# Kernel optimization log

Measured on AMD Instinct MI355X. Metric: run time of the kernel, lower is better.

Reference implementation:

```python
import jax, jax.numpy as jnp
import numpy as np

B, T, H, UNITS = 64, 512, 1024, 1024

def setup_inputs() -> dict:
    key = jax.random.key(0)
    ks = jax.random.split(key, 8)
    s = 0.02
    return {
        "dec_hidden": jax.random.normal(ks[0], (B, H), jnp.float32),
        "enc_output": jax.random.normal(ks[1], (B, T, H), jnp.float32),
        "Wh": jax.random.normal(ks[2], (H, UNITS), jnp.float32) * s,
        "bh": jnp.zeros((UNITS,), jnp.float32),
        "Ws": jax.random.normal(ks[3], (H, UNITS), jnp.float32) * s,
        "bs": jnp.zeros((UNITS,), jnp.float32),
        "Wv": jax.random.normal(ks[4], (UNITS, 1), jnp.float32) * s,
        "bv": jnp.zeros((1,), jnp.float32),
    }

def reference(dec_hidden, enc_output, Wh, bh, Ws, bs, Wv, bv):
    # Faithful to original: tanh applied only to W_h(enc_output) term.
    enc_proj = jnp.tanh(jnp.einsum('bth,hu->btu', enc_output, Wh) + bh)  # [B,T,U]
    dec_proj = (dec_hidden @ Ws + bs)[:, None, :]                        # [B,1,U]
    score = jnp.einsum('btu,uo->bto', enc_proj + dec_proj, Wv) + bv      # [B,T,1]
    attn_dist = jax.nn.softmax(score, axis=1)                            # [B,T,1]
    context_vector = jnp.sum(attn_dist * enc_output, axis=1)             # [B,H]
    return context_vector, jnp.squeeze(attn_dist, axis=-1)
```

## Files before the change

### kernel.cpp

```cpp
#include <hip/hip_runtime.h>
#include <hip/hip_bf16.h>

typedef unsigned short u16;
typedef __attribute__((ext_vector_type(8))) short short8;
typedef __attribute__((ext_vector_type(4))) float f32x4;

#define B_  64
#define T_  512
#define H_  1024
#define U_  1024
#define BT_ (B_*T_)

#define BM 128
#define BN 128
#define BK 32

#define GLL16(gp, lp) __builtin_amdgcn_global_load_lds( \
    (const __attribute__((address_space(1))) void*)(gp), \
    (__attribute__((address_space(3))) void*)(lp), 16, 0, 0)

__device__ __forceinline__ u16 f32_to_bf16(float f) {
  union { float f; unsigned u; } v; v.f = f;
  unsigned r = v.u + 0x7FFFu + ((v.u >> 16) & 1u);
  return (u16)(r >> 16);
}
__device__ __forceinline__ unsigned pack_bf16x2(float lo, float hi) {
  return (unsigned)f32_to_bf16(lo) | ((unsigned)f32_to_bf16(hi) << 16);
}

__global__ __launch_bounds__(256) void ba_conv_enc(const float4* __restrict__ in,
                                                   uint4* __restrict__ out) {
  int i = blockIdx.x * 256 + threadIdx.x;
  float4 v0 = in[2 * i], v1 = in[2 * i + 1];
  uint4 o;
  o.x = pack_bf16x2(v0.x, v0.y);
  o.y = pack_bf16x2(v0.z, v0.w);
  o.z = pack_bf16x2(v1.x, v1.y);
  o.w = pack_bf16x2(v1.z, v1.w);
  out[i] = o;
}

__global__ __launch_bounds__(256) void ba_conv_whT(const float* __restrict__ wh,
                                                   u16* __restrict__ whT) {
  __shared__ float tile[32][33];
  int tx = threadIdx.x, ty = threadIdx.y;
  int u0 = blockIdx.x * 32, h0 = blockIdx.y * 32;
  #pragma unroll
  for (int i = 0; i < 32; i += 8)
    tile[ty + i][tx] = wh[(long)(h0 + ty + i) * U_ + u0 + tx];
  __syncthreads();
  #pragma unroll
  for (int i = 0; i < 32; i += 8)
    whT[(long)(u0 + ty + i) * H_ + h0 + tx] = f32_to_bf16(tile[tx][ty + i]);
}

__global__ __launch_bounds__(256, 4) void ba_score(
    const u16* __restrict__ A, const u16* __restrict__ Bt,
    const float* __restrict__ bh, const float* __restrict__ wv,
    float* __restrict__ score) {
  __shared__ u16 lA[2][BM * BK];
  __shared__ u16 lB[2][BN * BK];

  const int tid  = threadIdx.x;
  const int wid  = tid >> 6;
  const int lane = tid & 63;
  const int wm = wid >> 1, wn = wid & 1;
  const long row0  = (long)blockIdx.x * BM;
  const int  ncol0 = blockIdx.y * BN;

  const int c0 = 2 * wid, c1 = 2 * wid + 1;
  const int lsub = lane >> 2;
  const int csw = (((lane & 3) - ((lane >> 3) & 3)) & 3) * 8;

  const int fr = lane & 15;
  const int pofs = ((((lane >> 4) + ((lane >> 1) & 3)) & 3)) * 8;

  const u16* gA0 = A + (row0 + 16 * c0 + lsub) * H_ + csw;
  const u16* gA1 = A + (row0 + 16 * c1 + lsub) * H_ + csw;
  const u16* gB0 = Bt + (long)(ncol0 + 16 * c0 + lsub) * H_ + csw;
  const u16* gB1 = Bt + (long)(ncol0 + 16 * c1 + lsub) * H_ + csw;

  f32x4 acc[4][4];
  #pragma unroll
  for (int i = 0; i < 4; ++i)
    #pragma unroll
    for (int j = 0; j < 4; ++j) acc[i][j] = (f32x4){0.f, 0.f, 0.f, 0.f};

  GLL16(gA0, (char*)lA[0] + c0 * 1024);
  GLL16(gA1, (char*)lA[0] + c1 * 1024);
  GLL16(gB0, (char*)lB[0] + c0 * 1024);
  GLL16(gB1, (char*)lB[0] + c1 * 1024);
  __syncthreads();

  int cur = 0;
  for (int kt = 0; kt < H_; kt += BK) {
    if (kt + BK < H_) {
      const int nxt = cur ^ 1;
      GLL16(gA0 + kt + BK, (char*)lA[nxt] + c0 * 1024);
      GLL16(gA1 + kt + BK, (char*)lA[nxt] + c1 * 1024);
      GLL16(gB0 + kt + BK, (char*)lB[nxt] + c0 * 1024);
      GLL16(gB1 + kt + BK, (char*)lB[nxt] + c1 * 1024);
    }

    short8 av[4], bvv[4];
    #pragma unroll
    for (int i = 0; i < 4; ++i) {
      av[i]  = *(const short8*)&lA[cur][(wm * 64 + i * 16 + fr) * BK + pofs];
      bvv[i] = *(const short8*)&lB[cur][(wn * 64 + i * 16 + fr) * BK + pofs];
    }
    #pragma unroll
    for (int i = 0; i < 4; ++i)
      #pragma unroll
      for (int j = 0; j < 4; ++j)
        acc[i][j] = __builtin_amdgcn_mfma_f32_16x16x32_bf16(av[i], bvv[j], acc[i][j], 0, 0, 0);

    __syncthreads();
    cur ^= 1;
  }

  float sloc[4][4];
  #pragma unroll
  for (int i = 0; i < 4; ++i)
    #pragma unroll
    for (int r = 0; r < 4; ++r) sloc[i][r] = 0.f;

  #pragma unroll
  for (int j = 0; j < 4; ++j) {
    const int n = ncol0 + wn * 64 + j * 16 + fr;
    const float bhn = bh[n];
    const float wvn = wv[n];
    #pragma unroll
    for (int i = 0; i < 4; ++i) {
      #pragma unroll
      for (int r = 0; r < 4; ++r) {
        float x = acc[i][j][r] + bhn;
        float e = __expf(2.f * x);
        float t = 1.f - 2.f / (e + 1.f);
        sloc[i][r] += t * wvn;
      }
    }
  }

  #pragma unroll
  for (int i = 0; i < 4; ++i) {
    #pragma unroll
    for (int r = 0; r < 4; ++r) {
      float v = sloc[i][r];
      v += __shfl_xor(v, 1);
      v += __shfl_xor(v, 2);
      v += __shfl_xor(v, 4);
      v += __shfl_xor(v, 8);
      if ((lane & 15) == 0) {
        int m = wm * 64 + i * 16 + (lane >> 4) * 4 + r;
        atomicAdd(&score[row0 + m], v);
      }
    }
  }
}

__global__ __launch_bounds__(256) void ba_softmax(const float* __restrict__ score,
                                                  float* __restrict__ attn) {
  int b = blockIdx.x, tid = threadIdx.x;
  int lane = tid & 63, wid = tid >> 6;
  const float* s = score + b * T_;
  float v0 = s[tid], v1 = s[tid + 256];
  float m = fmaxf(v0, v1);
  #pragma unroll
  for (int o = 1; o < 64; o <<= 1) m = fmaxf(m, __shfl_xor(m, o));
  __shared__ float redm[4];
  __shared__ float reds[4];
  if (lane == 0) redm[wid] = m;
  __syncthreads();
  m = fmaxf(fmaxf(redm[0], redm[1]), fmaxf(redm[2], redm[3]));
  float e0 = __expf(v0 - m), e1 = __expf(v1 - m);
  float sum = e0 + e1;
  #pragma unroll
  for (int o = 1; o < 64; o <<= 1) sum += __shfl_xor(sum, o);
  if (lane == 0) reds[wid] = sum;
  __syncthreads();
  float tot = reds[0] + reds[1] + reds[2] + reds[3];
  float inv = 1.f / tot;
  attn[b * T_ + tid] = e0 * inv;
  attn[b * T_ + tid + 256] = e1 * inv;
}

__global__ __launch_bounds__(256) void ba_context1(const float4* __restrict__ enc4,
                                                   const float* __restrict__ attn,
                                                   float4* __restrict__ part) {
  int b = blockIdx.x;
  int c = blockIdx.y;
  int tid = threadIdx.x;
  const float4* e = enc4 + ((long)b * T_ + c * 32) * (H_ / 4) + tid;
  const float* a = attn + b * T_ + c * 32;
  float4 acc = {0.f, 0.f, 0.f, 0.f};
  #pragma unroll 4
  for (int t = 0; t < 32; ++t) {
    float4 v = e[(long)t * (H_ / 4)];
    float at = a[t];
    acc.x = fmaf(at, v.x, acc.x);
    acc.y = fmaf(at, v.y, acc.y);
    acc.z = fmaf(at, v.z, acc.z);
    acc.w = fmaf(at, v.w, acc.w);
  }
  part[((long)b * 16 + c) * (H_ / 4) + tid] = acc;
}

__global__ __launch_bounds__(256) void ba_context2(const float4* __restrict__ part,
                                                   float4* __restrict__ ctx) {
  int b = blockIdx.x;
  int tid = threadIdx.x;
  const float4* p = part + (long)b * 16 * (H_ / 4) + tid;
  float4 acc = {0.f, 0.f, 0.f, 0.f};
  #pragma unroll
  for (int c = 0; c < 16; ++c) {
    float4 v = p[c * (H_ / 4)];
    acc.x += v.x; acc.y += v.y; acc.z += v.z; acc.w += v.w;
  }
  ctx[b * (H_ / 4) + tid] = acc;
}

extern "C" void kernel_launch(void* const* d_in, const int* in_sizes, int n_in,
                              void* d_out, int out_size, void* d_ws, size_t ws_size,
                              hipStream_t stream) {
  const float* enc = (const float*)d_in[1];
  const float* Wh  = (const float*)d_in[2];
  const float* bh  = (const float*)d_in[3];
  const float* Wv  = (const float*)d_in[6];

  float* out      = (float*)d_out;
  float* ctx_out  = out;
  float* attn_out = out + B_ * H_;

  char* ws = (char*)d_ws;
  u16*   encb  = (u16*)ws;
  u16*   whT   = (u16*)(ws + (size_t)67108864);
  float* score = (float*)(ws + (size_t)67108864 + 2097152);
  float* part  = (float*)(ws + (size_t)67108864 + 2097152 + 131072);

  ba_conv_enc<<<BT_ * H_ / 8 / 256, 256, 0, stream>>>((const float4*)enc, (uint4*)encb);
  ba_conv_whT<<<dim3(U_ / 32, H_ / 32), dim3(32, 8), 0, stream>>>(Wh, whT);
  hipMemsetAsync(score, 0, BT_ * sizeof(float), stream);
  ba_score<<<dim3(BT_ / BM, U_ / BN), 256, 0, stream>>>(encb, whT, bh, Wv, score);
  ba_softmax<<<B_, 256, 0, stream>>>(score, attn_out);
  ba_context1<<<dim3(B_, 16), 256, 0, stream>>>((const float4*)enc, attn_out, (float4*)part);
  ba_context2<<<B_, 256, 0, stream>>>((const float4*)part, (float4*)ctx_out);
}
```

Measured before the change: 328.0 us.

## Fuse prep kernels, triple-buffer GEMM pipeline, fold softmax into context kernel

Merges the enc conversion, Wh transpose and score zeroing into one prep launch, replacing two kernels and a memset. The score GEMM moves from a double-buffered to a triple-buffered LDS pipeline, with explicit vmcnt waits and raw barriers, and the occupancy hint drops from 4 to 3 blocks. Softmax is folded into the context kernel: each block recomputes the row softmax and stages its 32 weights in shared memory, which removes a launch but repeats the softmax work 16 times per batch row.

```diff
diff --git a/kernel.cpp b/kernel.cpp
--- a/kernel.cpp
+++ b/kernel.cpp
@@ -19,6 +19,11 @@
     (const __attribute__((address_space(1))) void*)(gp), \
     (__attribute__((address_space(3))) void*)(lp), 16, 0, 0)
 
+template<int N>
+__device__ __forceinline__ void vwait() {
+  asm volatile("s_waitcnt vmcnt(%0)" :: "n"(N) : "memory");
+}
+
 __device__ __forceinline__ u16 f32_to_bf16(float f) {
   union { float f; unsigned u; } v; v.f = f;
   unsigned r = v.u + 0x7FFFu + ((v.u >> 16) & 1u);
@@ -28,38 +33,44 @@
   return (unsigned)f32_to_bf16(lo) | ((unsigned)f32_to_bf16(hi) << 16);
 }
 
-__global__ __launch_bounds__(256) void ba_conv_enc(const float4* __restrict__ in,
-                                                   uint4* __restrict__ out) {
-  int i = blockIdx.x * 256 + threadIdx.x;
-  float4 v0 = in[2 * i], v1 = in[2 * i + 1];
-  uint4 o;
-  o.x = pack_bf16x2(v0.x, v0.y);
-  o.y = pack_bf16x2(v0.z, v0.w);
-  o.z = pack_bf16x2(v1.x, v1.y);
-  o.w = pack_bf16x2(v1.z, v1.w);
-  out[i] = o;
-}
-
-__global__ __launch_bounds__(256) void ba_conv_whT(const float* __restrict__ wh,
-                                                   u16* __restrict__ whT) {
+__global__ __launch_bounds__(256) void ba_prep(const float4* __restrict__ in,
+                                               uint4* __restrict__ out,
+                                               const float* __restrict__ wh,
+                                               u16* __restrict__ whT,
+                                               float* __restrict__ score) {
   __shared__ float tile[32][33];
-  int tx = threadIdx.x, ty = threadIdx.y;
-  int u0 = blockIdx.x * 32, h0 = blockIdx.y * 32;
-  #pragma unroll
-  for (int i = 0; i < 32; i += 8)
-    tile[ty + i][tx] = wh[(long)(h0 + ty + i) * U_ + u0 + tx];
-  __syncthreads();
-  #pragma unroll
-  for (int i = 0; i < 32; i += 8)
-    whT[(long)(u0 + ty + i) * H_ + h0 + tx] = f32_to_bf16(tile[tx][ty + i]);
-}
-
-__global__ __launch_bounds__(256, 4) void ba_score(
+  const int bx = blockIdx.x;
+  const int tid = threadIdx.x;
+  if (bx < 16384) {
+    int i = bx * 256 + tid;
+    float4 v0 = in[2 * i], v1 = in[2 * i + 1];
+    uint4 o;
+    o.x = pack_bf16x2(v0.x, v0.y);
+    o.y = pack_bf16x2(v0.z, v0.w);
+    o.z = pack_bf16x2(v1.x, v1.y);
+    o.w = pack_bf16x2(v1.z, v1.w);
+    out[i] = o;
+    if (bx < 128) score[bx * 256 + tid] = 0.f;
+  } else {
+    int wb = bx - 16384;
+    int u0 = (wb & 31) * 32, h0 = (wb >> 5) * 32;
+    int tx = tid & 31, ty = tid >> 5;
+    #pragma unroll
+    for (int i = 0; i < 32; i += 8)
+      tile[ty + i][tx] = wh[(long)(h0 + ty + i) * U_ + u0 + tx];
+    __syncthreads();
+    #pragma unroll
+    for (int i = 0; i < 32; i += 8)
+      whT[(long)(u0 + ty + i) * H_ + h0 + tx] = f32_to_bf16(tile[tx][ty + i]);
+  }
+}
+
+__global__ __launch_bounds__(256, 3) void ba_score(
     const u16* __restrict__ A, const u16* __restrict__ Bt,
     const float* __restrict__ bh, const float* __restrict__ wv,
     float* __restrict__ score) {
-  __shared__ u16 lA[2][BM * BK];
-  __shared__ u16 lB[2][BN * BK];
+  __shared__ u16 lA[3][BM * BK];
+  __shared__ u16 lB[3][BN * BK];
 
   const int tid  = threadIdx.x;
   const int wid  = tid >> 6;
@@ -86,37 +97,50 @@
     #pragma unroll
     for (int j = 0; j < 4; ++j) acc[i][j] = (f32x4){0.f, 0.f, 0.f, 0.f};
 
-  GLL16(gA0, (char*)lA[0] + c0 * 1024);
-  GLL16(gA1, (char*)lA[0] + c1 * 1024);
-  GLL16(gB0, (char*)lB[0] + c0 * 1024);
-  GLL16(gB1, (char*)lB[0] + c1 * 1024);
-  __syncthreads();
-
-  int cur = 0;
-  for (int kt = 0; kt < H_; kt += BK) {
-    if (kt + BK < H_) {
-      const int nxt = cur ^ 1;
-      GLL16(gA0 + kt + BK, (char*)lA[nxt] + c0 * 1024);
-      GLL16(gA1 + kt + BK, (char*)lA[nxt] + c1 * 1024);
-      GLL16(gB0 + kt + BK, (char*)lB[nxt] + c0 * 1024);
-      GLL16(gB1 + kt + BK, (char*)lB[nxt] + c1 * 1024);
-    }
-
-    short8 av[4], bvv[4];
-    #pragma unroll
-    for (int i = 0; i < 4; ++i) {
-      av[i]  = *(const short8*)&lA[cur][(wm * 64 + i * 16 + fr) * BK + pofs];
-      bvv[i] = *(const short8*)&lB[cur][(wn * 64 + i * 16 + fr) * BK + pofs];
-    }
-    #pragma unroll
-    for (int i = 0; i < 4; ++i)
-      #pragma unroll
-      for (int j = 0; j < 4; ++j)
-        acc[i][j] = __builtin_amdgcn_mfma_f32_16x16x32_bf16(av[i], bvv[j], acc[i][j], 0, 0, 0);
-
-    __syncthreads();
-    cur ^= 1;
-  }
+#define STAGE(t, b) do { \
+    const int _k = (t) * BK; \
+    GLL16(gA0 + _k, (char*)lA[b] + c0 * 1024); \
+    GLL16(gA1 + _k, (char*)lA[b] + c1 * 1024); \
+    GLL16(gB0 + _k, (char*)lB[b] + c0 * 1024); \
+    GLL16(gB1 + _k, (char*)lB[b] + c1 * 1024); \
+  } while (0)
+
+#define KSTEP(s, bi, WAITN) do { \
+    vwait<WAITN>(); \
+    __builtin_amdgcn_sched_barrier(0); \
+    __builtin_amdgcn_s_barrier(); \
+    __builtin_amdgcn_sched_barrier(0); \
+    short8 av[4], bvv[4]; \
+    _Pragma("unroll") \
+    for (int i = 0; i < 4; ++i) { \
+      av[i]  = *(const short8*)&lA[bi][(wm * 64 + i * 16 + fr) * BK + pofs]; \
+      bvv[i] = *(const short8*)&lB[bi][(wn * 64 + i * 16 + fr) * BK + pofs]; \
+    } \
+    _Pragma("unroll") \
+    for (int i = 0; i < 4; ++i) \
+      _Pragma("unroll") \
+      for (int j = 0; j < 4; ++j) \
+        acc[i][j] = __builtin_amdgcn_mfma_f32_16x16x32_bf16(av[i], bvv[j], acc[i][j], 0, 0, 0); \
+    __builtin_amdgcn_sched_barrier(0); \
+    __builtin_amdgcn_s_barrier(); \
+    __builtin_amdgcn_sched_barrier(0); \
+    if ((s) + 3 < 32) STAGE((s) + 3, bi); \
+  } while (0)
+
+  STAGE(0, 0);
+  STAGE(1, 1);
+  STAGE(2, 2);
+
+  int bi = 0;
+  for (int s = 0; s < 30; ++s) {
+    KSTEP(s, bi, 8);
+    bi = (bi == 2) ? 0 : bi + 1;
+  }
+  KSTEP(30, bi, 4);
+  bi = (bi == 2) ? 0 : bi + 1;
+  KSTEP(31, bi, 0);
+#undef KSTEP
+#undef STAGE
 
   float sloc[4][4];
   #pragma unroll
@@ -158,17 +182,19 @@
   }
 }
 
-__global__ __launch_bounds__(256) void ba_softmax(const float* __restrict__ score,
-                                                  float* __restrict__ attn) {
-  int b = blockIdx.x, tid = threadIdx.x;
+__global__ __launch_bounds__(256) void ba_context1(const float4* __restrict__ enc4,
+                                                   const float* __restrict__ score,
+                                                   float* __restrict__ attn_out,
+                                                   float4* __restrict__ part) {
+  __shared__ float redm[4], reds[4];
+  __shared__ float atile[32];
+  int b = blockIdx.x, c = blockIdx.y, tid = threadIdx.x;
   int lane = tid & 63, wid = tid >> 6;
   const float* s = score + b * T_;
   float v0 = s[tid], v1 = s[tid + 256];
   float m = fmaxf(v0, v1);
   #pragma unroll
   for (int o = 1; o < 64; o <<= 1) m = fmaxf(m, __shfl_xor(m, o));
-  __shared__ float redm[4];
-  __shared__ float reds[4];
   if (lane == 0) redm[wid] = m;
   __syncthreads();
   m = fmaxf(fmaxf(redm[0], redm[1]), fmaxf(redm[2], redm[3]));
@@ -178,25 +204,27 @@
   for (int o = 1; o < 64; o <<= 1) sum += __shfl_xor(sum, o);
   if (lane == 0) reds[wid] = sum;
   __syncthreads();
-  float tot = reds[0] + reds[1] + reds[2] + reds[3];
-  float inv = 1.f / tot;
-  attn[b * T_ + tid] = e0 * inv;
-  attn[b * T_ + tid + 256] = e1 * inv;
-}
-
-__global__ __launch_bounds__(256) void ba_context1(const float4* __restrict__ enc4,
-                                                   const float* __restrict__ attn,
-                                                   float4* __restrict__ part) {
-  int b = blockIdx.x;
-  int c = blockIdx.y;
-  int tid = threadIdx.x;
-  const float4* e = enc4 + ((long)b * T_ + c * 32) * (H_ / 4) + tid;
-  const float* a = attn + b * T_ + c * 32;
+  float inv = 1.f / (reds[0] + reds[1] + reds[2] + reds[3]);
+
+  if (c == 0) {
+    attn_out[b * T_ + tid] = e0 * inv;
+    attn_out[b * T_ + tid + 256] = e1 * inv;
+  }
+  int base = c * 32;
+  if (base < 256) {
+    if (tid >= base && tid < base + 32) atile[tid - base] = e0 * inv;
+  } else {
+    int bb = base - 256;
+    if (tid >= bb && tid < bb + 32) atile[tid - bb] = e1 * inv;
+  }
+  __syncthreads();
+
+  const float4* e = enc4 + ((long)b * T_ + base) * (H_ / 4) + tid;
   float4 acc = {0.f, 0.f, 0.f, 0.f};
   #pragma unroll 4
   for (int t = 0; t < 32; ++t) {
     float4 v = e[(long)t * (H_ / 4)];
-    float at = a[t];
+    float at = atile[t];
     acc.x = fmaf(at, v.x, acc.x);
     acc.y = fmaf(at, v.y, acc.y);
     acc.z = fmaf(at, v.z, acc.z);
@@ -237,11 +265,10 @@
   float* score = (float*)(ws + (size_t)67108864 + 2097152);
   float* part  = (float*)(ws + (size_t)67108864 + 2097152 + 131072);
 
-  ba_conv_enc<<<BT_ * H_ / 8 / 256, 256, 0, stream>>>((const float4*)enc, (uint4*)encb);
-  ba_conv_whT<<<dim3(U_ / 32, H_ / 32), dim3(32, 8), 0, stream>>>(Wh, whT);
-  hipMemsetAsync(score, 0, BT_ * sizeof(float), stream);
+  ba_prep<<<16384 + 1024, 256, 0, stream>>>((const float4*)enc, (uint4*)encb,
+                                            Wh, whT, score);
   ba_score<<<dim3(BT_ / BM, U_ / BN), 256, 0, stream>>>(encb, whT, bh, Wv, score);
-  ba_softmax<<<B_, 256, 0, stream>>>(score, attn_out);
-  ba_context1<<<dim3(B_, 16), 256, 0, stream>>>((const float4*)enc, attn_out, (float4*)part);
+  ba_context1<<<dim3(B_, 16), 256, 0, stream>>>((const float4*)enc, score,
+                                                attn_out, (float4*)part);
   ba_context2<<<B_, 256, 0, stream>>>((const float4*)part, (float4*)ctx_out);
 }
```

New measurement: 323.1 us. No clear change (-1.5%).
